# Optimization experiments

Measured on AMD Instinct MI355X. Metric: run time of the kernel, lower is better.

Reference implementation:

```python
import jax, jax.numpy as jnp
import numpy as np
import math

D_MODEL = 1024
N_HEADS = 16
D_HEAD = 64
GROUP_SIZE = 2
N_GROUPS = N_HEADS // GROUP_SIZE
D_MLP = 4096
BATCH = 2
SEQ = 2048
LN_EPS = 1e-5


def setup_inputs() -> dict:
    key = jax.random.key(0)
    ks = jax.random.split(key, 12)

    def xavier(k, shape):
        # torch xavier_uniform on a 3D tensor treats dim0 as fan_in, prod(rest) as fan_out
        fan_in = shape[0]
        fan_out = int(np.prod(shape[1:]))
        bound = math.sqrt(6.0 / (fan_in + fan_out))
        return jax.random.uniform(k, shape, jnp.float32, -bound, bound)

    def linear_w(k, out_f, in_f):
        bound = 1.0 / math.sqrt(in_f)
        return jax.random.uniform(k, (out_f, in_f), jnp.float32, -bound, bound)

    return {
        "x": jax.random.normal(ks[0], (BATCH, SEQ, D_MODEL), jnp.float32),
        "ln1_w": jnp.ones((D_MODEL,), jnp.float32),
        "ln1_b": jnp.zeros((D_MODEL,), jnp.float32),
        "W_Q": xavier(ks[1], (D_MODEL, N_HEADS, D_HEAD)),
        "W_K": xavier(ks[2], (D_MODEL, N_GROUPS, D_HEAD)),
        "W_V": xavier(ks[3], (D_MODEL, N_GROUPS, D_HEAD)),
        "W_out": xavier(ks[4], (D_HEAD, N_HEADS, D_MODEL)),
        "b_out": jnp.zeros((D_MODEL,), jnp.float32),
        "ln2_w": jnp.ones((D_MODEL,), jnp.float32),
        "ln2_b": jnp.zeros((D_MODEL,), jnp.float32),
        "mlp1_w": linear_w(ks[5], D_MLP, D_MODEL),
        "mlp1_b": jax.random.uniform(ks[6], (D_MLP,), jnp.float32, -1.0 / math.sqrt(D_MODEL), 1.0 / math.sqrt(D_MODEL)),
        "mlp2_w": linear_w(ks[7], D_MODEL, D_MLP),
        "mlp2_b": jax.random.uniform(ks[8], (D_MODEL,), jnp.float32, -1.0 / math.sqrt(D_MLP), 1.0 / math.sqrt(D_MLP)),
    }


def _layernorm(x, w, b):
    mu = jnp.mean(x, axis=-1, keepdims=True)
    var = jnp.var(x, axis=-1, keepdims=True)
    return (x - mu) * jax.lax.rsqrt(var + LN_EPS) * w + b


def _gqa_attention(resid, W_Q, W_K, W_V, W_out, b_out):
    b, s, _ = resid.shape
    q = jnp.einsum("bsd,dhk->bshk", resid, W_Q)            # [b, s, n_heads, d_head]
    q = q.reshape(b, s, N_GROUPS, GROUP_SIZE, D_HEAD)      # [b, s, g, gs, k]
    k = jnp.einsum("bsd,dgk->bsgk", resid, W_K)            # [b, s, g, k]
    v = jnp.einsum("bsd,dgk->bsgk", resid, W_V)
    scores = jnp.einsum("bqgik,btgk->bgiqt", q, k) / math.sqrt(D_HEAD)  # [b, g, gs, q, t]
    causal_mask = jnp.triu(jnp.ones((s, s), dtype=bool), k=1)
    scores = jnp.where(causal_mask, jnp.float32(-1000000.0), scores)
    probs = jax.nn.softmax(scores, axis=-1)
    z = jnp.einsum("bgiqt,btgk->bqgik", probs, v)          # [b, q, g, gs, k]
    z = z.reshape(b, s, N_HEADS, D_HEAD)
    return jnp.einsum("bshk,khd->bsd", z, W_out) + b_out


def reference(x, ln1_w, ln1_b, W_Q, W_K, W_V, W_out, b_out,
              ln2_w, ln2_b, mlp1_w, mlp1_b, mlp2_w, mlp2_b):
    normed = _layernorm(x, ln1_w, ln1_b)
    attn_out = _gqa_attention(normed, W_Q, W_K, W_V, W_out, b_out)
    post_attn = x + attn_out
    h = _layernorm(post_attn, ln2_w, ln2_b)
    h = jax.nn.gelu(h @ mlp1_w.T + mlp1_b, approximate=False)  # torch nn.GELU default = exact erf
    mlp_out = h @ mlp2_w.T + mlp2_b
    return post_attn + mlp_out
```

## Files before the change

### kernel.cpp

```cpp
#include <hip/hip_runtime.h>
#include <cstdint>
#include <cstddef>

typedef __attribute__((ext_vector_type(8))) short short8;
typedef __attribute__((ext_vector_type(4))) float f32x4;
typedef unsigned short u16;

#define MFMA16(a, b, c) __builtin_amdgcn_mfma_f32_16x16x32_bf16((a), (b), (c), 0, 0, 0)
#define SCL2 0.18033688011112042f

__device__ __forceinline__ u16 f2bf(float f) {
  union { float f; unsigned u; } c; c.f = f;
  unsigned r = c.u + 0x7fffu + ((c.u >> 16) & 1u);
  return (u16)(r >> 16);
}

__device__ __forceinline__ float bf2f(u16 x) {
  union { unsigned u; float f; } c; c.u = ((unsigned)x) << 16;
  return c.f;
}

__device__ __forceinline__ unsigned cvtpk(float a, float b) {
  unsigned r;
  asm("v_cvt_pk_bf16_f32 %0, %1, %2" : "=v"(r) : "v"(a), "v"(b));
  return r;
}


__global__ __launch_bounds__(256) void prep_wqkv(const float* __restrict__ wq,
    const float* __restrict__ wk, const float* __restrict__ wv, u16* __restrict__ outp)
{
  __shared__ float t[32][33];
  const int tx = threadIdx.x & 31, ty = threadIdx.x >> 5;
  const int n0 = blockIdx.x * 32, d0 = blockIdx.y * 32;
  const float* src; int stride, nc;
  if (n0 < 1024)      { src = wq; stride = 1024; nc = n0; }
  else if (n0 < 1536) { src = wk; stride = 512;  nc = n0 - 1024; }
  else                { src = wv; stride = 512;  nc = n0 - 1536; }
#pragma unroll
  for (int i = 0; i < 32; i += 8)
    t[ty + i][tx] = src[(size_t)(d0 + ty + i) * stride + nc + tx];
  __syncthreads();
#pragma unroll
  for (int i = 0; i < 32; i += 8)
    outp[(size_t)(n0 + ty + i) * 1024 + d0 + tx] = f2bf(t[tx][ty + i]);
}

__global__ __launch_bounds__(256) void prep_wout(const float* __restrict__ wo, u16* __restrict__ outp)
{
  __shared__ float t[32][33];
  const int tx = threadIdx.x & 31, ty = threadIdx.x >> 5;
  const int d0 = blockIdx.x * 32, c0 = blockIdx.y * 32;
#pragma unroll
  for (int i = 0; i < 32; i += 8) {
    int c = c0 + ty + i;
    t[ty + i][tx] = wo[(size_t)(c & 63) * 16384 + (size_t)(c >> 6) * 1024 + d0 + tx];
  }
  __syncthreads();
#pragma unroll
  for (int i = 0; i < 32; i += 8)
    outp[(size_t)(d0 + ty + i) * 1024 + c0 + tx] = f2bf(t[tx][ty + i]);
}

__global__ void convert_bf16(const float4* __restrict__ in, u16* __restrict__ out, int n4) {
  int i = blockIdx.x * 256 + threadIdx.x;
  if (i >= n4) return;
  float4 v = in[i];
  ushort4 o; o.x = f2bf(v.x); o.y = f2bf(v.y); o.z = f2bf(v.z); o.w = f2bf(v.w);
  ((ushort4*)out)[i] = o;
}

__global__ __launch_bounds__(256) void vt_transpose(const u16* __restrict__ qkv, u16* __restrict__ vtp)
{
  __shared__ u16 t[32][33];
  const int tx = threadIdx.x & 31, ty = threadIdx.x >> 5;
  const int t0 = blockIdx.x * 32, k0 = blockIdx.y * 32;
  const int bg = blockIdx.z, b = bg >> 3, g = bg & 7;
#pragma unroll
  for (int i = 0; i < 32; i += 8)
    t[ty + i][tx] = qkv[(size_t)(b * 2048 + t0 + ty + i) * 2048 + 1536 + g * 64 + k0 + tx];
  __syncthreads();
#pragma unroll
  for (int i = 0; i < 32; i += 8)
    vtp[(size_t)(bg * 64 + k0 + ty + i) * 2048 + t0 + tx] = t[tx][ty + i];
}

__global__ __launch_bounds__(256) void ln_bf16(const float* __restrict__ x,
    const float* __restrict__ w, const float* __restrict__ b, u16* __restrict__ out)
{
  const int row = blockIdx.x, tid = threadIdx.x;
  const float4 v = ((const float4*)(x + (size_t)row * 1024))[tid];
  float s = v.x + v.y + v.z + v.w;
  float s2 = v.x * v.x + v.y * v.y + v.z * v.z + v.w * v.w;
#pragma unroll
  for (int m = 32; m >= 1; m >>= 1) { s += __shfl_xor(s, m); s2 += __shfl_xor(s2, m); }
  __shared__ float red[8];
  if ((tid & 63) == 0) { red[tid >> 6] = s; red[4 + (tid >> 6)] = s2; }
  __syncthreads();
  s  = red[0] + red[1] + red[2] + red[3];
  s2 = red[4] + red[5] + red[6] + red[7];
  const float mu = s * (1.f / 1024.f);
  const float inv = rsqrtf(s2 * (1.f / 1024.f) - mu * mu + 1e-5f);
  const float4 wv = ((const float4*)w)[tid];
  const float4 bv = ((const float4*)b)[tid];
  ushort4 o;
  o.x = f2bf((v.x - mu) * inv * wv.x + bv.x);
  o.y = f2bf((v.y - mu) * inv * wv.y + bv.y);
  o.z = f2bf((v.z - mu) * inv * wv.z + bv.z);
  o.w = f2bf((v.w - mu) * inv * wv.w + bv.w);
  ((ushort4*)out)[(size_t)row * 256 + tid] = o;
}

#define BM 128
#define BN 128
#define BK 32

template<int EPI>
__global__ __launch_bounds__(256, 2) void gemm_bt(
    const u16* __restrict__ A, const u16* __restrict__ Bt, void* __restrict__ Cout,
    const float* __restrict__ bias, const float* __restrict__ resid,
    int M, int N, int K)
{
  __shared__ u16 As[4][BM * BK];
  __shared__ u16 Bs[4][BN * BK];
  const int tid = threadIdx.x;
  const int w = tid >> 6, lane = tid & 63;
  const int lo = lane & 15, hi = lane >> 4;
  const int mBase = blockIdx.x * BM, nBase = blockIdx.y * BN;
  const int wr = (w >> 1) * 64, wc = (w & 1) * 64;

  const f32x4 vzero = {0.f, 0.f, 0.f, 0.f};
  f32x4 acc[4][4];
#pragma unroll
  for (int i = 0; i < 4; ++i)
#pragma unroll
    for (int j = 0; j < 4; ++j) acc[i][j] = vzero;

  const int base0 = w * 2048 + lane * 16;
  int srow[2], skb[2];
#pragma unroll
  for (int c = 0; c < 2; ++c) {
    const int off = base0 + c * 1024;
    srow[c] = off >> 6;
    skb[c] = (off & 63) >> 1;
  }

  const int NT = K >> 5;

  auto stage = [&](int kt) {
    const int slot = kt & 3;
    const int k0 = kt * BK;
#pragma unroll
    for (int c = 0; c < 2; ++c) {
      const u16* ga = A  + (size_t)(mBase + srow[c]) * K + k0 + skb[c];
      const u16* gb = Bt + (size_t)(nBase + srow[c]) * K + k0 + skb[c];
      __builtin_amdgcn_global_load_lds((const __attribute__((address_space(1))) void*)ga,
          (__attribute__((address_space(3))) void*)((char*)&As[slot][0] + w * 2048 + c * 1024), 16, 0, 0);
      __builtin_amdgcn_global_load_lds((const __attribute__((address_space(1))) void*)gb,
          (__attribute__((address_space(3))) void*)((char*)&Bs[slot][0] + w * 2048 + c * 1024), 16, 0, 0);
    }
  };

  stage(0);
  stage(1);

  for (int kt = 0; kt < NT; ++kt) {
    if (kt + 2 < NT) {
      stage(kt + 2);
      asm volatile("s_waitcnt vmcnt(8)" ::: "memory");
    } else if (kt + 1 < NT) {
      asm volatile("s_waitcnt vmcnt(4)" ::: "memory");
    } else {
      asm volatile("s_waitcnt vmcnt(0)" ::: "memory");
    }
    __builtin_amdgcn_s_barrier();
    __builtin_amdgcn_sched_barrier(0);

    const int slot = kt & 3;
    short8 af[4], bf[4];
#pragma unroll
    for (int i = 0; i < 4; ++i) {
      af[i] = *(const short8*)((const char*)&As[slot][0] + (wr + i * 16 + lo) * 64 + hi * 16);
      bf[i] = *(const short8*)((const char*)&Bs[slot][0] + (wc + i * 16 + lo) * 64 + hi * 16);
    }
    __builtin_amdgcn_s_setprio(1);
#pragma unroll
    for (int i = 0; i < 4; ++i)
#pragma unroll
      for (int j = 0; j < 4; ++j)
        acc[i][j] = MFMA16(af[i], bf[j], acc[i][j]);
    __builtin_amdgcn_s_setprio(0);
  }

#pragma unroll
  for (int i = 0; i < 4; ++i) {
#pragma unroll
    for (int j = 0; j < 4; ++j) {
#pragma unroll
      for (int r = 0; r < 4; ++r) {
        const int row = mBase + wr + i * 16 + hi * 4 + r;
        const int col = nBase + wc + j * 16 + lo;
        float v = acc[i][j][r];
        if (EPI == 3 && col < 1024) v *= SCL2;
        ((u16*)Cout)[(size_t)row * N + col] = f2bf(v);
      }
    }
  }
}

template<int EPI>
__global__ __launch_bounds__(256, 3) void gemm_n64(
    const u16* __restrict__ A, const u16* __restrict__ Bt, void* __restrict__ Cout,
    const float* __restrict__ bias, const float* __restrict__ resid,
    int M, int N, int K)
{
  __shared__ u16 As[4][128 * 32];
  __shared__ u16 Bs[4][64 * 32];
  const int tid = threadIdx.x;
  const int w = tid >> 6, lane = tid & 63;
  const int lo = lane & 15, hi = lane >> 4;
  const int mBase = blockIdx.x * 128, nBase = blockIdx.y * 64;
  const int wr = (w >> 1) * 64, wc = (w & 1) * 32;

  const f32x4 vzero = {0.f, 0.f, 0.f, 0.f};
  f32x4 acc[4][2];
#pragma unroll
  for (int i = 0; i < 4; ++i)
#pragma unroll
    for (int j = 0; j < 2; ++j) acc[i][j] = vzero;

  int arow[2], akb[2];
#pragma unroll
  for (int c = 0; c < 2; ++c) {
    const int off = tid * 16 + c * 4096;
    arow[c] = off >> 6;
    akb[c] = (off & 63) >> 1;
  }
  const int brow = (tid * 16) >> 6, bkb = ((tid * 16) & 63) >> 1;

  const int NT = K >> 5;

  auto stage = [&](int kt) {
    const int slot = kt & 3;
    const int k0 = kt * 32;
#pragma unroll
    for (int c = 0; c < 2; ++c) {
      const u16* ga = A + (size_t)(mBase + arow[c]) * K + k0 + akb[c];
      __builtin_amdgcn_global_load_lds((const __attribute__((address_space(1))) void*)ga,
          (__attribute__((address_space(3))) void*)((char*)&As[slot][0] + tid * 16 + c * 4096), 16, 0, 0);
    }
    const u16* gb = Bt + (size_t)(nBase + brow) * K + k0 + bkb;
    __builtin_amdgcn_global_load_lds((const __attribute__((address_space(1))) void*)gb,
        (__attribute__((address_space(3))) void*)((char*)&Bs[slot][0] + tid * 16), 16, 0, 0);
  };

  stage(0);
  stage(1);

  for (int kt = 0; kt < NT; ++kt) {
    if (kt + 2 < NT) {
      stage(kt + 2);
      asm volatile("s_waitcnt vmcnt(6)" ::: "memory");
    } else if (kt + 1 < NT) {
      asm volatile("s_waitcnt vmcnt(3)" ::: "memory");
    } else {
      asm volatile("s_waitcnt vmcnt(0)" ::: "memory");
    }
    __builtin_amdgcn_s_barrier();
    __builtin_amdgcn_sched_barrier(0);

    const int slot = kt & 3;
    short8 af[4], bf[2];
#pragma unroll
    for (int i = 0; i < 4; ++i)
      af[i] = *(const short8*)((const char*)&As[slot][0] + (wr + i * 16 + lo) * 64 + hi * 16);
#pragma unroll
    for (int j = 0; j < 2; ++j)
      bf[j] = *(const short8*)((const char*)&Bs[slot][0] + (wc + j * 16 + lo) * 64 + hi * 16);
    __builtin_amdgcn_s_setprio(1);
#pragma unroll
    for (int i = 0; i < 4; ++i)
#pragma unroll
      for (int j = 0; j < 2; ++j)
        acc[i][j] = MFMA16(af[i], bf[j], acc[i][j]);
    __builtin_amdgcn_s_setprio(0);
  }

#pragma unroll
  for (int i = 0; i < 4; ++i) {
#pragma unroll
    for (int j = 0; j < 2; ++j) {
#pragma unroll
      for (int r = 0; r < 4; ++r) {
        const int row = mBase + wr + i * 16 + hi * 4 + r;
        const int col = nBase + wc + j * 16 + lo;
        float v = acc[i][j][r];
        v += bias[col];
        v += resid[(size_t)row * N + col];
        ((float*)Cout)[(size_t)row * N + col] = v;
      }
    }
  }
}

template<int EPI>
__global__ __launch_bounds__(512, 2) void gemm256(
    const u16* __restrict__ A, const u16* __restrict__ Bt, void* __restrict__ Cout,
    const float* __restrict__ bias, const float* __restrict__ resid,
    int M, int N, int K)
{
  __shared__ u16 lds8[2][2][2][8192];
  const int tid = threadIdx.x;
  const int lane = tid & 63, lo = lane & 15, hi = lane >> 4;
  const int wid = tid >> 6, wr = wid >> 2, wc = wid & 3;
  const int mBase = blockIdx.x * 256, nBase = blockIdx.y * 256;
  const int sw = (lo & 7) << 4;

  const f32x4 vzero = {0.f, 0.f, 0.f, 0.f};
  f32x4 acc[8][4];
#pragma unroll
  for (int i = 0; i < 8; ++i)
#pragma unroll
    for (int j = 0; j < 4; ++j) acc[i][j] = vzero;

  int srow[2], scol[2];
#pragma unroll
  for (int c = 0; c < 2; ++c) {
    const int p = c * 8192 + tid * 16;
    const int r = p >> 7, bb = p & 127;
    srow[c] = r;
    scol[c] = (bb ^ ((r & 7) << 4)) >> 1;
  }

  const int NT = K >> 6;

#pragma unroll
  for (int mat = 0; mat < 2; ++mat)
#pragma unroll
    for (int half = 0; half < 2; ++half)
#pragma unroll
      for (int c = 0; c < 2; ++c) {
        const u16* g = (mat == 0)
          ? A  + (size_t)(mBase + half * 128 + srow[c]) * K + scol[c]
          : Bt + (size_t)(nBase + half * 128 + srow[c]) * K + scol[c];
        __builtin_amdgcn_global_load_lds((const __attribute__((address_space(1))) void*)g,
            (__attribute__((address_space(3))) void*)(&lds8[0][mat][half][c * 4096 + tid * 8]), 16, 0, 0);
      }
  asm volatile("s_waitcnt vmcnt(0)" ::: "memory");
  asm volatile("s_barrier" ::: "memory");

  for (int kt = 0; kt < NT; ++kt) {
    const int cur = kt & 1;
    const char* baseA = (const char*)&lds8[cur][0][wr][0];
    const char* baseB = (const char*)&lds8[cur][1][wc >> 1][0];
    const int rBB = (wc & 1) * 64;

    short8 bfr[4][2], afr[4][2];
#pragma unroll
    for (int nf = 0; nf < 4; ++nf)
#pragma unroll
      for (int ks = 0; ks < 2; ++ks)
        bfr[nf][ks] = *(const short8*)(baseB + (rBB + nf * 16 + lo) * 128 + ((ks * 64 + hi * 16) ^ sw));
#pragma unroll
    for (int mf = 0; mf < 4; ++mf)
#pragma unroll
      for (int ks = 0; ks < 2; ++ks)
        afr[mf][ks] = *(const short8*)(baseA + ((mf * 16 + lo) * 128 + ((ks * 64 + hi * 16) ^ sw)));

    if (kt + 1 < NT) {
      const int ko = (kt + 1) * 64;
#pragma unroll
      for (int mat = 0; mat < 2; ++mat)
#pragma unroll
        for (int half = 0; half < 2; ++half)
#pragma unroll
          for (int c = 0; c < 2; ++c) {
            const u16* g = (mat == 0)
              ? A  + (size_t)(mBase + half * 128 + srow[c]) * K + ko + scol[c]
              : Bt + (size_t)(nBase + half * 128 + srow[c]) * K + ko + scol[c];
            __builtin_amdgcn_global_load_lds((const __attribute__((address_space(1))) void*)g,
                (__attribute__((address_space(3))) void*)(&lds8[cur ^ 1][mat][half][c * 4096 + tid * 8]), 16, 0, 0);
          }
    }

    __builtin_amdgcn_s_setprio(1);
#pragma unroll
    for (int mf = 0; mf < 4; ++mf)
#pragma unroll
      for (int nf = 0; nf < 4; ++nf)
#pragma unroll
        for (int ks = 0; ks < 2; ++ks)
          acc[mf][nf] = MFMA16(afr[mf][ks], bfr[nf][ks], acc[mf][nf]);
    __builtin_amdgcn_s_setprio(0);

#pragma unroll
    for (int mf = 0; mf < 4; ++mf)
#pragma unroll
      for (int ks = 0; ks < 2; ++ks)
        afr[mf][ks] = *(const short8*)(baseA + (((mf + 4) * 16 + lo) * 128 + ((ks * 64 + hi * 16) ^ sw)));

    __builtin_amdgcn_s_setprio(1);
#pragma unroll
    for (int mf = 0; mf < 4; ++mf)
#pragma unroll
      for (int nf = 0; nf < 4; ++nf)
#pragma unroll
        for (int ks = 0; ks < 2; ++ks)
          acc[mf + 4][nf] = MFMA16(afr[mf][ks], bfr[nf][ks], acc[mf + 4][nf]);
    __builtin_amdgcn_s_setprio(0);

    asm volatile("s_waitcnt vmcnt(0)" ::: "memory");
    asm volatile("s_barrier" ::: "memory");
  }

#pragma unroll
  for (int mf = 0; mf < 8; ++mf) {
#pragma unroll
    for (int nf = 0; nf < 4; ++nf) {
#pragma unroll
      for (int r = 0; r < 4; ++r) {
        const int row = mBase + wr * 128 + mf * 16 + hi * 4 + r;
        const int col = nBase + wc * 64 + nf * 16 + lo;
        float v = acc[mf][nf][r];
        if (EPI != 0) v += bias[col];
        if (EPI == 1) v += resid[(size_t)row * N + col];
        if (EPI == 2) v = 0.5f * v * (1.f + erff(v * 0.70710678118f));
        if (EPI == 1) ((float*)Cout)[(size_t)row * N + col] = v;
        else          ((u16*)Cout)[(size_t)row * N + col] = f2bf(v);
      }
    }
  }
}

__global__ __launch_bounds__(256) void attn_fwd(const u16* __restrict__ qkv,
    const u16* __restrict__ vt, u16* __restrict__ z,
    u16* __restrict__ zscr, float* __restrict__ lscr)
{
  __shared__ u16 Ks[2][64 * 64];
  __shared__ u16 Vs[2][64 * 64];
  __shared__ u16 Pl[4][32 * 72];
  const int tid = threadIdx.x;
  const int w = tid >> 6, lane = tid & 63, lo = lane & 15, hi = lane >> 4;
  const int bx = blockIdx.x;
  int chunk, itBeg, itEnd, mode;
  if (bx < 16)      { chunk = bx;      itBeg = 0;  itEnd = chunk + 1; mode = 0; }
  else if (bx < 32) { chunk = bx;      itBeg = 0;  itEnd = 16;        mode = 1; }
  else              { chunk = bx - 16; itBeg = 16; itEnd = chunk + 1; mode = 2; }
  const int bg = blockIdx.y, b = bg >> 3, g = bg & 7;
  const int h = (g << 1) | (w & 1);
  const int q0w = chunk * 64 + (w >> 1) * 32;
  const int sw = (lo & 7) << 4;

  short8 qA[2][2];
#pragma unroll
  for (int qf = 0; qf < 2; ++qf)
#pragma unroll
    for (int half = 0; half < 2; ++half)
      qA[qf][half] = *(const short8*)(qkv +
          (size_t)(b * 2048 + q0w + qf * 16 + lo) * 2048 + h * 64 + half * 32 + hi * 8);

  const f32x4 vzero = {0.f, 0.f, 0.f, 0.f};
  f32x4 zacc[2][4];
#pragma unroll
  for (int qf = 0; qf < 2; ++qf)
#pragma unroll
    for (int kf = 0; kf < 4; ++kf) zacc[qf][kf] = vzero;
  float lrun[2] = {0.f, 0.f};

  const u16* kbase = qkv + (size_t)b * 2048 * 2048 + 1024 + g * 64;
  const u16* vbase = vt + (size_t)(b * 8 + g) * 64 * 2048;

  int srow[2], scol[2];
#pragma unroll
  for (int c = 0; c < 2; ++c) {
    const int p = tid * 16 + c * 4096;
    const int r = p >> 7, bb = p & 127;
    srow[c] = r;
    scol[c] = (bb ^ ((r & 7) << 4)) >> 1;
  }

  u16* pw = &Pl[w][0];

  auto stageKV = [&](int it) {
    const int slot = it & 1;
    const int t0 = it * 64;
#pragma unroll
    for (int c = 0; c < 2; ++c) {
      __builtin_amdgcn_global_load_lds(
          (const __attribute__((address_space(1))) void*)(kbase + (size_t)(t0 + srow[c]) * 2048 + scol[c]),
          (__attribute__((address_space(3))) void*)((char*)&Ks[slot][0] + tid * 16 + c * 4096), 16, 0, 0);
      __builtin_amdgcn_global_load_lds(
          (const __attribute__((address_space(1))) void*)(vbase + (size_t)srow[c] * 2048 + t0 + scol[c]),
          (__attribute__((address_space(3))) void*)((char*)&Vs[slot][0] + tid * 16 + c * 4096), 16, 0, 0);
    }
  };

  stageKV(itBeg);

  for (int it = itBeg; it < itEnd; ++it) {
    asm volatile("s_waitcnt vmcnt(0)" ::: "memory");
    __builtin_amdgcn_s_barrier();
    __builtin_amdgcn_sched_barrier(0);
    if (it + 1 < itEnd) stageKV(it + 1);

    const int slot = it & 1;
    const int ts = it * 64;
    const char* KsB = (const char*)&Ks[slot][0];
    const char* VsB = (const char*)&Vs[slot][0];

    short8 kA[4][2];
#pragma unroll
    for (int nt = 0; nt < 4; ++nt)
#pragma unroll
      for (int half = 0; half < 2; ++half)
        kA[nt][half] = *(const short8*)(KsB + (nt * 16 + lo) * 128 + ((half * 64 + hi * 16) ^ sw));

#pragma unroll
    for (int qf = 0; qf < 2; ++qf) {
      f32x4 p[4];
#pragma unroll
      for (int nt = 0; nt < 4; ++nt) {
        f32x4 t = MFMA16(kA[nt][0], qA[qf][0], vzero);
        p[nt] = MFMA16(kA[nt][1], qA[qf][1], t);
      }
      const int qrow0 = q0w + qf * 16;
      if (ts + 63 > qrow0) {
        const int rel = qrow0 + lo - ts;
#pragma unroll
        for (int nt = 0; nt < 4; ++nt)
#pragma unroll
          for (int r = 0; r < 4; ++r)
            if (nt * 16 + hi * 4 + r > rel) p[nt][r] = -1e30f;
      }
#pragma unroll
      for (int nt = 0; nt < 4; ++nt)
#pragma unroll
        for (int r = 0; r < 4; ++r) p[nt][r] = exp2f(p[nt][r]);
      float s0 = (p[0][0] + p[0][1]) + (p[0][2] + p[0][3]);
      float s1 = (p[1][0] + p[1][1]) + (p[1][2] + p[1][3]);
      float s2 = (p[2][0] + p[2][1]) + (p[2][2] + p[2][3]);
      float s3 = (p[3][0] + p[3][1]) + (p[3][2] + p[3][3]);
      lrun[qf] += (s0 + s1) + (s2 + s3);
#pragma unroll
      for (int nt = 0; nt < 4; ++nt) {
        uint2 uu;
        uu.x = cvtpk(p[nt][0], p[nt][1]);
        uu.y = cvtpk(p[nt][2], p[nt][3]);
        *(uint2*)((char*)pw + (qf * 16 + lo) * 144 + nt * 32 + hi * 8) = uu;
      }
    }
    asm volatile("s_waitcnt lgkmcnt(0)" ::: "memory");
    short8 pa[2][2];
#pragma unroll
    for (int qf = 0; qf < 2; ++qf)
#pragma unroll
      for (int tc = 0; tc < 2; ++tc)
        pa[qf][tc] = *(const short8*)((const char*)pw + (qf * 16 + lo) * 144 + tc * 64 + hi * 16);
#pragma unroll
    for (int kf = 0; kf < 4; ++kf) {
#pragma unroll
      for (int tc = 0; tc < 2; ++tc) {
        const short8 vf = *(const short8*)(VsB + (kf * 16 + lo) * 128 + ((tc * 64 + hi * 16) ^ sw));
        zacc[0][kf] = MFMA16(vf, pa[0][tc], zacc[0][kf]);
        zacc[1][kf] = MFMA16(vf, pa[1][tc], zacc[1][kf]);
      }
    }
  }

  if (mode == 0) {
    u16* zp = z + (size_t)(b * 2048 + q0w) * 1024 + h * 64;
#pragma unroll
    for (int qf = 0; qf < 2; ++qf) {
      float rs = lrun[qf];
      rs += __shfl_xor(rs, 16);
      rs += __shfl_xor(rs, 32);
      const float inv = 1.f / rs;
#pragma unroll
      for (int kf = 0; kf < 4; ++kf) {
        uint2 o;
        o.x = cvtpk(zacc[qf][kf][0] * inv, zacc[qf][kf][1] * inv);
        o.y = cvtpk(zacc[qf][kf][2] * inv, zacc[qf][kf][3] * inv);
        *(uint2*)(zp + (size_t)(qf * 16 + lo) * 1024 + kf * 16 + hi * 4) = o;
      }
    }
  } else {
    const int seg = mode - 1;
    const int ci = chunk - 16;
    const int idx2 = (bg * 16 + ci) * 2 + (w & 1);
    u16* zs = zscr + ((size_t)seg * 512 * 4096) + ((size_t)idx2 * 64 + (w >> 1) * 32) * 64;
    float* ls = lscr + (size_t)seg * 512 * 64 + (size_t)idx2 * 64 + (w >> 1) * 32;
#pragma unroll
    for (int qf = 0; qf < 2; ++qf) {
      float rs = lrun[qf];
      rs += __shfl_xor(rs, 16);
      rs += __shfl_xor(rs, 32);
      if (hi == 0) ls[qf * 16 + lo] = rs;
#pragma unroll
      for (int kf = 0; kf < 4; ++kf) {
        uint2 o;
        o.x = cvtpk(zacc[qf][kf][0], zacc[qf][kf][1]);
        o.y = cvtpk(zacc[qf][kf][2], zacc[qf][kf][3]);
        *(uint2*)(zs + (size_t)(qf * 16 + lo) * 64 + kf * 16 + hi * 4) = o;
      }
    }
  }
}

__global__ __launch_bounds__(256) void attn_combine(const u16* __restrict__ zscr,
    const float* __restrict__ lscr, u16* __restrict__ z)
{
  const int bgci = blockIdx.x;
  const int bg = bgci >> 4, ci = bgci & 15;
  const int b = bg >> 3, g = bg & 7, chunk = 16 + ci;
  const int tid = threadIdx.x;
#pragma unroll
  for (int j = 0; j < 4; ++j) {
    const int v = tid + j * 256;
    const int k8 = v & 7, row = (v >> 3) & 63, hh = v >> 9;
    const size_t base = ((size_t)(bgci * 2 + hh) * 64 + row) * 64 + k8 * 8;
    const short8 z0 = *(const short8*)(zscr + base);
    const short8 z1 = *(const short8*)(zscr + (size_t)512 * 4096 + base);
    const size_t lidx = (size_t)(bgci * 2 + hh) * 64 + row;
    const float inv = 1.f / (lscr[lidx] + lscr[(size_t)512 * 64 + lidx]);
    float a[8];
#pragma unroll
    for (int e = 0; e < 8; ++e)
      a[e] = (bf2f((u16)z0[e]) + bf2f((u16)z1[e])) * inv;
    uint4 o;
    o.x = cvtpk(a[0], a[1]);
    o.y = cvtpk(a[2], a[3]);
    o.z = cvtpk(a[4], a[5]);
    o.w = cvtpk(a[6], a[7]);
    *(uint4*)(z + ((size_t)(b * 2048 + chunk * 64 + row)) * 1024 + (g * 2 + hh) * 64 + k8 * 8) = o;
  }
}


extern "C" void kernel_launch(void* const* d_in, const int* in_sizes, int n_in,
                              void* d_out, int out_size, void* d_ws, size_t ws_size,
                              hipStream_t stream)
{
  (void)in_sizes; (void)n_in; (void)out_size; (void)ws_size;
  const float* x      = (const float*)d_in[0];
  const float* ln1_w  = (const float*)d_in[1];
  const float* ln1_b  = (const float*)d_in[2];
  const float* W_Q    = (const float*)d_in[3];
  const float* W_K    = (const float*)d_in[4];
  const float* W_V    = (const float*)d_in[5];
  const float* W_out  = (const float*)d_in[6];
  const float* b_out  = (const float*)d_in[7];
  const float* ln2_w  = (const float*)d_in[8];
  const float* ln2_b  = (const float*)d_in[9];
  const float* mlp1_w = (const float*)d_in[10];
  const float* mlp1_b = (const float*)d_in[11];
  const float* mlp2_w = (const float*)d_in[12];
  const float* mlp2_b = (const float*)d_in[13];
  float* out = (float*)d_out;

  char* ws = (char*)d_ws;
  u16*   wqkv_t = (u16*)(ws + 0);
  u16*   wout_t = (u16*)(ws + 4194304);
  u16*   w1     = (u16*)(ws + 6291456);
  u16*   w2     = (u16*)(ws + 14680064);
  u16*   normed = (u16*)(ws + 23068672);
  float* post   = (float*)(ws + 31457280);
  u16*   qkv    = (u16*)(ws + 48234496);
  u16*   vtb    = (u16*)(ws + 65011712);
  u16*   zb     = (u16*)(ws + 69206016);
  u16*   hbuf   = (u16*)(ws + 48234496);
  u16*   zscr   = (u16*)(ws + 31457280);
  float* lscr   = (float*)(ws + 23068672);

  prep_wqkv<<<dim3(64, 32), 256, 0, stream>>>(W_Q, W_K, W_V, wqkv_t);
  prep_wout<<<dim3(32, 32), 256, 0, stream>>>(W_out, wout_t);
  convert_bf16<<<4096, 256, 0, stream>>>((const float4*)mlp1_w, w1, 1048576);
  convert_bf16<<<4096, 256, 0, stream>>>((const float4*)mlp2_w, w2, 1048576);

  ln_bf16<<<4096, 256, 0, stream>>>(x, ln1_w, ln1_b, normed);
  gemm_bt<3><<<dim3(32, 16), 256, 0, stream>>>(normed, wqkv_t, qkv, nullptr, nullptr, 4096, 2048, 1024);
  vt_transpose<<<dim3(64, 2, 16), 256, 0, stream>>>(qkv, vtb);
  attn_fwd<<<dim3(48, 16), 256, 0, stream>>>(qkv, vtb, zb, zscr, lscr);
  attn_combine<<<256, 256, 0, stream>>>(zscr, lscr, zb);
  gemm_n64<1><<<dim3(32, 16), 256, 0, stream>>>(zb, wout_t, post, b_out, x, 4096, 1024, 1024);
  ln_bf16<<<4096, 256, 0, stream>>>(post, ln2_w, ln2_b, normed);
  gemm256<2><<<dim3(16, 16), 512, 0, stream>>>(normed, w1, hbuf, mlp1_b, nullptr, 4096, 4096, 1024);
  gemm_n64<1><<<dim3(32, 16), 256, 0, stream>>>(hbuf, w2, out, mlp2_b, post, 4096, 1024, 4096);
}
```

Baseline: 248.6 us.

## Split-K the MLP2 GEMM into two halves with a bf16 partial combine kernel

The MLP down-projection (K=4096) now runs as a split-K GEMM across two z-slices. Each slice writes bf16 partial sums into reused workspace buffers, and a new combine kernel adds the partials, bias and residual. The aim is to double the grid from 512 blocks, raising occupancy across the CUs and shortening the long serial K loop. In exchange it adds an extra kernel launch and partial-buffer traffic, and rounding each partial to bf16 before summing costs some accuracy.

```diff
diff --git a/kernel.cpp b/kernel.cpp
--- a/kernel.cpp
+++ b/kernel.cpp
@@ -210,9 +210,10 @@
 
 template<int EPI>
 __global__ __launch_bounds__(256, 3) void gemm_n64(
-    const u16* __restrict__ A, const u16* __restrict__ Bt, void* __restrict__ Cout,
+    const u16* __restrict__ A, const u16* __restrict__ Bt,
+    void* __restrict__ Cout, void* __restrict__ Cout2,
     const float* __restrict__ bias, const float* __restrict__ resid,
-    int M, int N, int K)
+    int M, int N, int K, int Ks)
 {
   __shared__ u16 As[4][128 * 32];
   __shared__ u16 Bs[4][64 * 32];
@@ -221,6 +222,8 @@
   const int lo = lane & 15, hi = lane >> 4;
   const int mBase = blockIdx.x * 128, nBase = blockIdx.y * 64;
   const int wr = (w >> 1) * 64, wc = (w & 1) * 32;
+  const int kOff = blockIdx.z * K;
+  A += kOff; Bt += kOff;
 
   const f32x4 vzero = {0.f, 0.f, 0.f, 0.f};
   f32x4 acc[4][2];
@@ -245,11 +248,11 @@
     const int k0 = kt * 32;
 #pragma unroll
     for (int c = 0; c < 2; ++c) {
-      const u16* ga = A + (size_t)(mBase + arow[c]) * K + k0 + akb[c];
+      const u16* ga = A + (size_t)(mBase + arow[c]) * Ks + k0 + akb[c];
       __builtin_amdgcn_global_load_lds((const __attribute__((address_space(1))) void*)ga,
           (__attribute__((address_space(3))) void*)((char*)&As[slot][0] + tid * 16 + c * 4096), 16, 0, 0);
     }
-    const u16* gb = Bt + (size_t)(nBase + brow) * K + k0 + bkb;
+    const u16* gb = Bt + (size_t)(nBase + brow) * Ks + k0 + bkb;
     __builtin_amdgcn_global_load_lds((const __attribute__((address_space(1))) void*)gb,
         (__attribute__((address_space(3))) void*)((char*)&Bs[slot][0] + tid * 16), 16, 0, 0);
   };
@@ -286,6 +289,7 @@
     __builtin_amdgcn_s_setprio(0);
   }
 
+  void* sel = (EPI == 4 && blockIdx.z) ? Cout2 : Cout;
 #pragma unroll
   for (int i = 0; i < 4; ++i) {
 #pragma unroll
@@ -295,11 +299,38 @@
         const int row = mBase + wr + i * 16 + hi * 4 + r;
         const int col = nBase + wc + j * 16 + lo;
         float v = acc[i][j][r];
-        v += bias[col];
-        v += resid[(size_t)row * N + col];
-        ((float*)Cout)[(size_t)row * N + col] = v;
-      }
-    }
+        if (EPI == 1) {
+          v += bias[col];
+          v += resid[(size_t)row * N + col];
+          ((float*)sel)[(size_t)row * N + col] = v;
+        } else {
+          ((u16*)sel)[(size_t)row * N + col] = f2bf(v);
+        }
+      }
+    }
+  }
+}
+
+__global__ __launch_bounds__(256) void mlp2_combine(const u16* __restrict__ p0,
+    const u16* __restrict__ p1, const float* __restrict__ bias,
+    const float* __restrict__ resid, float* __restrict__ out)
+{
+  const int tid = threadIdx.x;
+  const int c0 = tid * 4;
+  const float4 bv = *(const float4*)(bias + c0);
+#pragma unroll
+  for (int rr = 0; rr < 4; ++rr) {
+    const int row = blockIdx.x * 4 + rr;
+    const size_t off = (size_t)row * 1024 + c0;
+    const ushort4 a = *(const ushort4*)(p0 + off);
+    const ushort4 b = *(const ushort4*)(p1 + off);
+    const float4 rv = *(const float4*)(resid + off);
+    float4 o;
+    o.x = bf2f(a.x) + bf2f(b.x) + bv.x + rv.x;
+    o.y = bf2f(a.y) + bf2f(b.y) + bv.y + rv.y;
+    o.z = bf2f(a.z) + bf2f(b.z) + bv.z + rv.z;
+    o.w = bf2f(a.w) + bf2f(b.w) + bv.w + rv.w;
+    *(float4*)(out + off) = o;
   }
 }
 
@@ -670,6 +701,8 @@
   u16*   hbuf   = (u16*)(ws + 48234496);
   u16*   zscr   = (u16*)(ws + 31457280);
   float* lscr   = (float*)(ws + 23068672);
+  u16*   mp0    = (u16*)(ws + 0);
+  u16*   mp1    = (u16*)(ws + 23068672);
 
   prep_wqkv<<<dim3(64, 32), 256, 0, stream>>>(W_Q, W_K, W_V, wqkv_t);
   prep_wout<<<dim3(32, 32), 256, 0, stream>>>(W_out, wout_t);
@@ -681,8 +714,9 @@
   vt_transpose<<<dim3(64, 2, 16), 256, 0, stream>>>(qkv, vtb);
   attn_fwd<<<dim3(48, 16), 256, 0, stream>>>(qkv, vtb, zb, zscr, lscr);
   attn_combine<<<256, 256, 0, stream>>>(zscr, lscr, zb);
-  gemm_n64<1><<<dim3(32, 16), 256, 0, stream>>>(zb, wout_t, post, b_out, x, 4096, 1024, 1024);
+  gemm_n64<1><<<dim3(32, 16), 256, 0, stream>>>(zb, wout_t, post, nullptr, b_out, x, 4096, 1024, 1024, 1024);
   ln_bf16<<<4096, 256, 0, stream>>>(post, ln2_w, ln2_b, normed);
   gemm256<2><<<dim3(16, 16), 512, 0, stream>>>(normed, w1, hbuf, mlp1_b, nullptr, 4096, 4096, 1024);
-  gemm_n64<1><<<dim3(32, 16), 256, 0, stream>>>(hbuf, w2, out, mlp2_b, post, 4096, 1024, 4096);
-}
+  gemm_n64<4><<<dim3(32, 16, 2), 256, 0, stream>>>(hbuf, w2, mp0, mp1, nullptr, nullptr, 4096, 1024, 2048, 4096);
+  mlp2_combine<<<1024, 256, 0, stream>>>(mp0, mp1, mlp2_b, post, out);
+}
```

New measurement: 260.0 us. 1.05x slower.
